# Kernel optimization log

Measured on AMD Instinct MI355X. Metric: run time of the kernel, lower is better.

The kernel has to match this reference:

```python
import jax, jax.numpy as jnp
import numpy as np

SHAPE = (192, 224, 192)
COG = np.array([96.0, 112.0, 96.0], dtype=np.float32)


def _rotation(a):
    # a: (3,) angles. R = Rx @ Ry @ Rz, matching _compute_rotation.
    one = jnp.ones(()); zero = jnp.zeros(())
    cx, sx = jnp.cos(a[0]), jnp.sin(a[0])
    cy, sy = jnp.cos(a[1]), jnp.sin(a[1])
    cz, sz = jnp.cos(a[2]), jnp.sin(a[2])
    Rx = jnp.stack([jnp.stack([one, zero, zero]),
                    jnp.stack([zero, cx, -sx]),
                    jnp.stack([zero, sx, cx])])
    Ry = jnp.stack([jnp.stack([cy, zero, sy]),
                    jnp.stack([zero, one, zero]),
                    jnp.stack([-sy, zero, cy])])
    Rz = jnp.stack([jnp.stack([cz, -sz, zero]),
                    jnp.stack([sz, cz, zero]),
                    jnp.stack([zero, zero, one])])
    return Rx @ Ry @ Rz


def _compose_matrix(angle, translation, scaling, ref_v2r, flo_v2r):
    # factors are all 1; scaling param is log-scale -> exp
    ang = angle[0]
    sc = jnp.exp(scaling[0])
    tx = translation[0]
    eye = jnp.eye(4, dtype=angle.dtype)
    cog = jnp.asarray(COG, dtype=angle.dtype)
    T_center = eye.at[:3, 3].set(-cog)
    T_center_inv = eye.at[:3, 3].set(cog)
    T_sc = jnp.diag(jnp.concatenate([sc, jnp.ones((1,), angle.dtype)]))
    T_trans = eye.at[:3, 3].set(tx)
    T_rot = eye.at[:3, :3].set(_rotation(ang))
    T_rig = T_center_inv @ T_trans @ T_rot @ T_sc @ T_center
    return jnp.linalg.inv(flo_v2r) @ T_rig @ ref_v2r


def _trilinear(vol, di, dj, dk):
    # fast_3D_interp_torch, mode='linear': zero outside, clamp ceil at border
    D, H, W = vol.shape
    ok = (di > 0) & (dj > 0) & (dk > 0) & (di <= D - 1) & (dj <= H - 1) & (dk <= W - 1)
    fi = jnp.clip(jnp.floor(di), 0, D - 1)
    fj = jnp.clip(jnp.floor(dj), 0, H - 1)
    fk = jnp.clip(jnp.floor(dk), 0, W - 1)
    wi = di - fi; wj = dj - fj; wk = dk - fk
    fi = fi.astype(jnp.int32); fj = fj.astype(jnp.int32); fk = fk.astype(jnp.int32)
    ci = jnp.minimum(fi + 1, D - 1)
    cj = jnp.minimum(fj + 1, H - 1)
    ck = jnp.minimum(fk + 1, W - 1)
    c000 = vol[fi, fj, fk]; c100 = vol[ci, fj, fk]
    c010 = vol[fi, cj, fk]; c110 = vol[ci, cj, fk]
    c001 = vol[fi, fj, ck]; c101 = vol[ci, fj, ck]
    c011 = vol[fi, cj, ck]; c111 = vol[ci, cj, ck]
    out = ((c000 * (1 - wi) + c100 * wi) * (1 - wj) + (c010 * (1 - wi) + c110 * wi) * wj) * (1 - wk) \
        + ((c001 * (1 - wi) + c101 * wi) * (1 - wj) + (c011 * (1 - wi) + c111 * wi) * wj) * wk
    return jnp.where(ok, out, jnp.zeros((), vol.dtype))


def reference(image_targ, angle, translation, scaling, ref_v2r, flo_v2r):
    T = _compose_matrix(angle, translation, scaling, ref_v2r, flo_v2r)
    D, H, W = SHAPE
    ii, jj, kk = jnp.meshgrid(jnp.arange(D, dtype=image_targ.dtype),
                              jnp.arange(H, dtype=image_targ.dtype),
                              jnp.arange(W, dtype=image_targ.dtype), indexing='ij')
    di = T[0, 0] * ii + T[0, 1] * jj + T[0, 2] * kk + T[0, 3]
    dj = T[1, 0] * ii + T[1, 1] * jj + T[1, 2] * kk + T[1, 3]
    dk = T[2, 0] * ii + T[2, 1] * jj + T[2, 2] * kk + T[2, 3]
    out = _trilinear(image_targ[0, 0], di, dj, dk)
    return out[None, None]


def setup_inputs() -> dict:
    key = jax.random.key(0)
    k1, k2, k3, k4 = jax.random.split(key, 4)
    D, H, W = SHAPE
    image_targ = jax.random.normal(k1, (1, 1, D, H, W), dtype=jnp.float32)
    angle = jax.random.normal(k2, (1, 3), dtype=jnp.float32) * 0.05
    translation = jax.random.normal(k3, (1, 3), dtype=jnp.float32) * 2.0
    scaling = jax.random.normal(k4, (1, 3), dtype=jnp.float32) * 0.02
    ref_v2r = jnp.eye(4, dtype=jnp.float32)
    flo_v2r = jnp.eye(4, dtype=jnp.float32)
    return {"image_targ": image_targ, "angle": angle, "translation": translation,
            "scaling": scaling, "ref_v2r": ref_v2r, "flo_v2r": flo_v2r}
```

## Files before the change

### kernel.cpp

```cpp
#include <hip/hip_runtime.h>
#include <hip/hip_bf16.h>
#include <math.h>

#define D_DIM 192
#define H_DIM 224
#define W_DIM 192


__device__ inline void mm4(const float* A, const float* B, float* C) {
    for (int r = 0; r < 4; ++r)
        for (int c = 0; c < 4; ++c) {
            float s = 0.f;
            for (int t = 0; t < 4; ++t) s += A[r * 4 + t] * B[t * 4 + c];
            C[r * 4 + c] = s;
        }
}

__device__ inline void inv4(const float* Ain, float* out) {
    float a[4][8];
    for (int r = 0; r < 4; ++r) {
        for (int c = 0; c < 4; ++c) a[r][c] = Ain[r * 4 + c];
        for (int c = 0; c < 4; ++c) a[r][4 + c] = (r == c) ? 1.f : 0.f;
    }
    for (int col = 0; col < 4; ++col) {
        int piv = col;
        float best = fabsf(a[col][col]);
        for (int r = col + 1; r < 4; ++r) {
            float v = fabsf(a[r][col]);
            if (v > best) { best = v; piv = r; }
        }
        if (piv != col) {
            for (int c = 0; c < 8; ++c) {
                float t = a[col][c]; a[col][c] = a[piv][c]; a[piv][c] = t;
            }
        }
        float inv = 1.f / a[col][col];
        for (int c = 0; c < 8; ++c) a[col][c] *= inv;
        for (int r = 0; r < 4; ++r) {
            if (r == col) continue;
            float f = a[r][col];
            for (int c = 0; c < 8; ++c) a[r][c] -= f * a[col][c];
        }
    }
    for (int r = 0; r < 4; ++r)
        for (int c = 0; c < 4; ++c) out[r * 4 + c] = a[r][4 + c];
}

__global__ void compute_T_kernel(const float* __restrict__ ang,
                                 const float* __restrict__ tr,
                                 const float* __restrict__ scl,
                                 const float* __restrict__ ref_v2r,
                                 const float* __restrict__ flo_v2r,
                                 float* __restrict__ Tout) {
    if (threadIdx.x != 0 || blockIdx.x != 0) return;

    const float cogx = 96.f, cogy = 112.f, cogz = 96.f;

    float cx = cosf(ang[0]), sx = sinf(ang[0]);
    float cy = cosf(ang[1]), sy = sinf(ang[1]);
    float cz = cosf(ang[2]), sz = sinf(ang[2]);

    float Rx[9] = {1, 0, 0, 0, cx, -sx, 0, sx, cx};
    float Ry[9] = {cy, 0, sy, 0, 1, 0, -sy, 0, cy};
    float Rz[9] = {cz, -sz, 0, sz, cz, 0, 0, 0, 1};
    float Ryz[9], R[9];
    for (int r = 0; r < 3; ++r)
        for (int c = 0; c < 3; ++c) {
            float s = 0.f;
            for (int t = 0; t < 3; ++t) s += Ry[r * 3 + t] * Rz[t * 3 + c];
            Ryz[r * 3 + c] = s;
        }
    for (int r = 0; r < 3; ++r)
        for (int c = 0; c < 3; ++c) {
            float s = 0.f;
            for (int t = 0; t < 3; ++t) s += Rx[r * 3 + t] * Ryz[t * 3 + c];
            R[r * 3 + c] = s;
        }

    float s0 = expf(scl[0]), s1 = expf(scl[1]), s2 = expf(scl[2]);

    float Tc[16]    = {1,0,0,-cogx, 0,1,0,-cogy, 0,0,1,-cogz, 0,0,0,1};
    float Tci[16]   = {1,0,0, cogx, 0,1,0, cogy, 0,0,1, cogz, 0,0,0,1};
    float Tsc[16]   = {s0,0,0,0, 0,s1,0,0, 0,0,s2,0, 0,0,0,1};
    float Ttr[16]   = {1,0,0,tr[0], 0,1,0,tr[1], 0,0,1,tr[2], 0,0,0,1};
    float Trot[16]  = {R[0],R[1],R[2],0, R[3],R[4],R[5],0, R[6],R[7],R[8],0, 0,0,0,1};

    float m1[16], m2[16], m3[16], Trig[16];
    mm4(Tci, Ttr, m1);
    mm4(m1, Trot, m2);
    mm4(m2, Tsc, m3);
    mm4(m3, Tc, Trig);

    float floinv[16], m4[16], T[16];
    inv4(flo_v2r, floinv);
    mm4(floinv, Trig, m4);
    mm4(m4, ref_v2r, T);

    for (int q = 0; q < 12; ++q) Tout[q] = T[q];
}


__global__ __launch_bounds__(W_DIM) void resample_kernel(
    const float* __restrict__ vol,
    const float* __restrict__ T,
    float* __restrict__ out) {
    const int k = threadIdx.x;
    const int j = blockIdx.y;
    const int i = blockIdx.z;

    const float fi = (float)i, fj = (float)j, fk = (float)k;

    const float t00 = T[0],  t01 = T[1],  t02 = T[2],  t03 = T[3];
    const float t10 = T[4],  t11 = T[5],  t12 = T[6],  t13 = T[7];
    const float t20 = T[8],  t21 = T[9],  t22 = T[10], t23 = T[11];

    const float di = t00 * fi + t01 * fj + t02 * fk + t03;
    const float dj = t10 * fi + t11 * fj + t12 * fk + t13;
    const float dk = t20 * fi + t21 * fj + t22 * fk + t23;

    const bool ok = (di > 0.f) & (dj > 0.f) & (dk > 0.f) &
                    (di <= (float)(D_DIM - 1)) &
                    (dj <= (float)(H_DIM - 1)) &
                    (dk <= (float)(W_DIM - 1));

    float ffi = fminf(fmaxf(floorf(di), 0.f), (float)(D_DIM - 1));
    float ffj = fminf(fmaxf(floorf(dj), 0.f), (float)(H_DIM - 1));
    float ffk = fminf(fmaxf(floorf(dk), 0.f), (float)(W_DIM - 1));

    const float wi = di - ffi;
    const float wj = dj - ffj;
    const float wk = dk - ffk;

    const int i0 = (int)ffi, j0 = (int)ffj, k0 = (int)ffk;
    const int i1 = min(i0 + 1, D_DIM - 1);
    const int j1 = min(j0 + 1, H_DIM - 1);
    const int k1 = min(k0 + 1, W_DIM - 1);

    const int base00 = (i0 * H_DIM + j0) * W_DIM;
    const int base01 = (i0 * H_DIM + j1) * W_DIM;
    const int base10 = (i1 * H_DIM + j0) * W_DIM;
    const int base11 = (i1 * H_DIM + j1) * W_DIM;

    const float c000 = vol[base00 + k0];
    const float c100 = vol[base10 + k0];
    const float c010 = vol[base01 + k0];
    const float c110 = vol[base11 + k0];
    const float c001 = vol[base00 + k1];
    const float c101 = vol[base10 + k1];
    const float c011 = vol[base01 + k1];
    const float c111 = vol[base11 + k1];

    const float omwi = 1.f - wi, omwj = 1.f - wj, omwk = 1.f - wk;

    const float v = ((c000 * omwi + c100 * wi) * omwj +
                     (c010 * omwi + c110 * wi) * wj) * omwk +
                    ((c001 * omwi + c101 * wi) * omwj +
                     (c011 * omwi + c111 * wi) * wj) * wk;

    out[(i * H_DIM + j) * W_DIM + k] = ok ? v : 0.f;
}


extern "C" void kernel_launch(void* const* d_in, const int* in_sizes, int n_in,
                              void* d_out, int out_size, void* d_ws, size_t ws_size,
                              hipStream_t stream) {
    const float* image_targ  = (const float*)d_in[0];
    const float* angle       = (const float*)d_in[1];
    const float* translation = (const float*)d_in[2];
    const float* scaling     = (const float*)d_in[3];
    const float* ref_v2r     = (const float*)d_in[4];
    const float* flo_v2r     = (const float*)d_in[5];
    float* out = (float*)d_out;
    float* Tmat = (float*)d_ws;

    compute_T_kernel<<<1, 1, 0, stream>>>(angle, translation, scaling,
                                          ref_v2r, flo_v2r, Tmat);

    dim3 block(W_DIM, 1, 1);
    dim3 grid(1, H_DIM, D_DIM);
    resample_kernel<<<grid, block, 0, stream>>>(image_targ, Tmat, out);
}
```

Baseline: 140.6 us.

## Process four rows per block with XCD-aware block remapping and nontemporal stores

Each block now handles four consecutive j-rows, issuing all 32 gather loads before the interpolation math so more memory requests are in flight per thread. Block indices are remapped so consecutive spatial chunks land on the same XCD, which is meant to improve L2 locality for neighbouring gather footprints. Output writes use nontemporal stores to avoid polluting cache. Register pressure rises and the total block count drops by four times.

```diff
diff --git a/kernel.cpp b/kernel.cpp
--- a/kernel.cpp
+++ b/kernel.cpp
@@ -5,6 +5,8 @@
 #define D_DIM 192
 #define H_DIM 224
 #define W_DIM 192
+#define ROWS_PER_BLOCK 4
+#define NUM_XCD 8
 
 
 __device__ inline void mm4(const float* A, const float* B, float* C) {
@@ -79,11 +81,11 @@
 
     float s0 = expf(scl[0]), s1 = expf(scl[1]), s2 = expf(scl[2]);
 
-    float Tc[16]    = {1,0,0,-cogx, 0,1,0,-cogy, 0,0,1,-cogz, 0,0,0,1};
-    float Tci[16]   = {1,0,0, cogx, 0,1,0, cogy, 0,0,1, cogz, 0,0,0,1};
-    float Tsc[16]   = {s0,0,0,0, 0,s1,0,0, 0,0,s2,0, 0,0,0,1};
-    float Ttr[16]   = {1,0,0,tr[0], 0,1,0,tr[1], 0,0,1,tr[2], 0,0,0,1};
-    float Trot[16]  = {R[0],R[1],R[2],0, R[3],R[4],R[5],0, R[6],R[7],R[8],0, 0,0,0,1};
+    float Tc[16]   = {1,0,0,-cogx, 0,1,0,-cogy, 0,0,1,-cogz, 0,0,0,1};
+    float Tci[16]  = {1,0,0, cogx, 0,1,0, cogy, 0,0,1, cogz, 0,0,0,1};
+    float Tsc[16]  = {s0,0,0,0, 0,s1,0,0, 0,0,s2,0, 0,0,0,1};
+    float Ttr[16]  = {1,0,0,tr[0], 0,1,0,tr[1], 0,0,1,tr[2], 0,0,0,1};
+    float Trot[16] = {R[0],R[1],R[2],0, R[3],R[4],R[5],0, R[6],R[7],R[8],0, 0,0,0,1};
 
     float m1[16], m2[16], m3[16], Trig[16];
     mm4(Tci, Ttr, m1);
@@ -104,60 +106,77 @@
     const float* __restrict__ vol,
     const float* __restrict__ T,
     float* __restrict__ out) {
+
+    constexpr int NBLK = (D_DIM * H_DIM) / ROWS_PER_BLOCK;
+    constexpr int PER_XCD = NBLK / NUM_XCD;
+
+    const int b = blockIdx.x;
+    const int xcd = b & (NUM_XCD - 1);
+    const int q = b >> 3;
+    const int sb = xcd * PER_XCD + q;
+    const int row_base = sb * ROWS_PER_BLOCK;
+    const int i = row_base / H_DIM;
+    const int jbase = row_base % H_DIM;
     const int k = threadIdx.x;
-    const int j = blockIdx.y;
-    const int i = blockIdx.z;
-
-    const float fi = (float)i, fj = (float)j, fk = (float)k;
 
     const float t00 = T[0],  t01 = T[1],  t02 = T[2],  t03 = T[3];
     const float t10 = T[4],  t11 = T[5],  t12 = T[6],  t13 = T[7];
     const float t20 = T[8],  t21 = T[9],  t22 = T[10], t23 = T[11];
 
-    const float di = t00 * fi + t01 * fj + t02 * fk + t03;
-    const float dj = t10 * fi + t11 * fj + t12 * fk + t13;
-    const float dk = t20 * fi + t21 * fj + t22 * fk + t23;
-
-    const bool ok = (di > 0.f) & (dj > 0.f) & (dk > 0.f) &
-                    (di <= (float)(D_DIM - 1)) &
-                    (dj <= (float)(H_DIM - 1)) &
-                    (dk <= (float)(W_DIM - 1));
-
-    float ffi = fminf(fmaxf(floorf(di), 0.f), (float)(D_DIM - 1));
-    float ffj = fminf(fmaxf(floorf(dj), 0.f), (float)(H_DIM - 1));
-    float ffk = fminf(fmaxf(floorf(dk), 0.f), (float)(W_DIM - 1));
-
-    const float wi = di - ffi;
-    const float wj = dj - ffj;
-    const float wk = dk - ffk;
-
-    const int i0 = (int)ffi, j0 = (int)ffj, k0 = (int)ffk;
-    const int i1 = min(i0 + 1, D_DIM - 1);
-    const int j1 = min(j0 + 1, H_DIM - 1);
-    const int k1 = min(k0 + 1, W_DIM - 1);
-
-    const int base00 = (i0 * H_DIM + j0) * W_DIM;
-    const int base01 = (i0 * H_DIM + j1) * W_DIM;
-    const int base10 = (i1 * H_DIM + j0) * W_DIM;
-    const int base11 = (i1 * H_DIM + j1) * W_DIM;
-
-    const float c000 = vol[base00 + k0];
-    const float c100 = vol[base10 + k0];
-    const float c010 = vol[base01 + k0];
-    const float c110 = vol[base11 + k0];
-    const float c001 = vol[base00 + k1];
-    const float c101 = vol[base10 + k1];
-    const float c011 = vol[base01 + k1];
-    const float c111 = vol[base11 + k1];
-
-    const float omwi = 1.f - wi, omwj = 1.f - wj, omwk = 1.f - wk;
-
-    const float v = ((c000 * omwi + c100 * wi) * omwj +
-                     (c010 * omwi + c110 * wi) * wj) * omwk +
-                    ((c001 * omwi + c101 * wi) * omwj +
-                     (c011 * omwi + c111 * wi) * wj) * wk;
-
-    out[(i * H_DIM + j) * W_DIM + k] = ok ? v : 0.f;
+    const float fi = (float)i, fk = (float)k;
+
+    float c[ROWS_PER_BLOCK][8];
+    float wi[ROWS_PER_BLOCK], wj[ROWS_PER_BLOCK], wk[ROWS_PER_BLOCK];
+    bool okr[ROWS_PER_BLOCK];
+
+#pragma unroll
+    for (int r = 0; r < ROWS_PER_BLOCK; ++r) {
+        const float fj = (float)(jbase + r);
+        const float di = t00 * fi + t01 * fj + t02 * fk + t03;
+        const float dj = t10 * fi + t11 * fj + t12 * fk + t13;
+        const float dk = t20 * fi + t21 * fj + t22 * fk + t23;
+
+        okr[r] = (di > 0.f) & (dj > 0.f) & (dk > 0.f) &
+                 (di <= (float)(D_DIM - 1)) &
+                 (dj <= (float)(H_DIM - 1)) &
+                 (dk <= (float)(W_DIM - 1));
+
+        float ffi = fminf(fmaxf(floorf(di), 0.f), (float)(D_DIM - 1));
+        float ffj = fminf(fmaxf(floorf(dj), 0.f), (float)(H_DIM - 1));
+        float ffk = fminf(fmaxf(floorf(dk), 0.f), (float)(W_DIM - 1));
+
+        wi[r] = di - ffi; wj[r] = dj - ffj; wk[r] = dk - ffk;
+
+        const int i0 = (int)ffi, j0 = (int)ffj, k0 = (int)ffk;
+        const int i1 = min(i0 + 1, D_DIM - 1);
+        const int j1 = min(j0 + 1, H_DIM - 1);
+        const int k1 = min(k0 + 1, W_DIM - 1);
+
+        const int base00 = (i0 * H_DIM + j0) * W_DIM;
+        const int base01 = (i0 * H_DIM + j1) * W_DIM;
+        const int base10 = (i1 * H_DIM + j0) * W_DIM;
+        const int base11 = (i1 * H_DIM + j1) * W_DIM;
+
+        c[r][0] = vol[base00 + k0];
+        c[r][1] = vol[base10 + k0];
+        c[r][2] = vol[base01 + k0];
+        c[r][3] = vol[base11 + k0];
+        c[r][4] = vol[base00 + k1];
+        c[r][5] = vol[base10 + k1];
+        c[r][6] = vol[base01 + k1];
+        c[r][7] = vol[base11 + k1];
+    }
+
+#pragma unroll
+    for (int r = 0; r < ROWS_PER_BLOCK; ++r) {
+        const float omwi = 1.f - wi[r], omwj = 1.f - wj[r], omwk = 1.f - wk[r];
+        const float v = ((c[r][0] * omwi + c[r][1] * wi[r]) * omwj +
+                         (c[r][2] * omwi + c[r][3] * wi[r]) * wj[r]) * omwk +
+                        ((c[r][4] * omwi + c[r][5] * wi[r]) * omwj +
+                         (c[r][6] * omwi + c[r][7] * wi[r]) * wj[r]) * wk[r];
+        const float res = okr[r] ? v : 0.f;
+        __builtin_nontemporal_store(res, &out[(i * H_DIM + (jbase + r)) * W_DIM + k]);
+    }
 }
 
 
@@ -176,7 +195,6 @@
     compute_T_kernel<<<1, 1, 0, stream>>>(angle, translation, scaling,
                                           ref_v2r, flo_v2r, Tmat);
 
-    dim3 block(W_DIM, 1, 1);
-    dim3 grid(1, H_DIM, D_DIM);
-    resample_kernel<<<grid, block, 0, stream>>>(image_targ, Tmat, out);
-}
+    const int nblk = (D_DIM * H_DIM) / ROWS_PER_BLOCK;
+    resample_kernel<<<nblk, W_DIM, 0, stream>>>(image_targ, Tmat, out);
+}
```

After: 142.8 us. Within noise of the previous version (+1.6%).

## Tile resampling into 3D blocks with shared-memory source staging and XCD-aware mapping

Applied to the files above, without the earlier changes.

Replaces the one-row-per-block trilinear resample with 8x8x16 output tiles of 256 threads. Each tile's source bounding box is computed from its corners and staged into LDS, so the eight neighbour gathers read shared memory instead of global memory, with a global-memory fallback when the box does not fit. Blocks are remapped so neighbouring tiles land on the same XCD for L2 locality, and outputs use nontemporal stores. This adds LDS staging cost and a barrier per tile, and loads some source voxels the tile never uses.

```diff
diff --git a/kernel.cpp b/kernel.cpp
--- a/kernel.cpp
+++ b/kernel.cpp
@@ -5,6 +5,13 @@
 #define D_DIM 192
 #define H_DIM 224
 #define W_DIM 192
+#define IT 8
+#define JT 8
+#define KT 16
+#define BLOCK 256
+#define NUM_XCD 8
+#define NKP 24
+#define MAXROWS 256
 
 
 __device__ inline void mm4(const float* A, const float* B, float* C) {
@@ -79,11 +86,11 @@
 
     float s0 = expf(scl[0]), s1 = expf(scl[1]), s2 = expf(scl[2]);
 
-    float Tc[16]    = {1,0,0,-cogx, 0,1,0,-cogy, 0,0,1,-cogz, 0,0,0,1};
-    float Tci[16]   = {1,0,0, cogx, 0,1,0, cogy, 0,0,1, cogz, 0,0,0,1};
-    float Tsc[16]   = {s0,0,0,0, 0,s1,0,0, 0,0,s2,0, 0,0,0,1};
-    float Ttr[16]   = {1,0,0,tr[0], 0,1,0,tr[1], 0,0,1,tr[2], 0,0,0,1};
-    float Trot[16]  = {R[0],R[1],R[2],0, R[3],R[4],R[5],0, R[6],R[7],R[8],0, 0,0,0,1};
+    float Tc[16]   = {1,0,0,-cogx, 0,1,0,-cogy, 0,0,1,-cogz, 0,0,0,1};
+    float Tci[16]  = {1,0,0, cogx, 0,1,0, cogy, 0,0,1, cogz, 0,0,0,1};
+    float Tsc[16]  = {s0,0,0,0, 0,s1,0,0, 0,0,s2,0, 0,0,0,1};
+    float Ttr[16]  = {1,0,0,tr[0], 0,1,0,tr[1], 0,0,1,tr[2], 0,0,0,1};
+    float Trot[16] = {R[0],R[1],R[2],0, R[3],R[4],R[5],0, R[6],R[7],R[8],0, 0,0,0,1};
 
     float m1[16], m2[16], m3[16], Trig[16];
     mm4(Tci, Ttr, m1);
@@ -100,64 +107,139 @@
 }
 
 
-__global__ __launch_bounds__(W_DIM) void resample_kernel(
+__global__ __launch_bounds__(BLOCK) void resample_kernel(
     const float* __restrict__ vol,
     const float* __restrict__ T,
     float* __restrict__ out) {
-    const int k = threadIdx.x;
-    const int j = blockIdx.y;
-    const int i = blockIdx.z;
-
-    const float fi = (float)i, fj = (float)j, fk = (float)k;
+
+    constexpr int NTI = D_DIM / IT;
+    constexpr int NTJ = H_DIM / JT;
+    constexpr int NTK = W_DIM / KT;
+    constexpr int NBLK = NTI * NTJ * NTK;
+    constexpr int PER_XCD = NBLK / NUM_XCD;
+
+    __shared__ float S[MAXROWS * NKP];
+
+    const int b = blockIdx.x;
+    const int xcd = b & (NUM_XCD - 1);
+    const int sb = xcd * PER_XCD + (b >> 3);
+    const int it = sb / (NTJ * NTK);
+    const int rem = sb - it * (NTJ * NTK);
+    const int jt = rem / NTK;
+    const int kt = rem - jt * NTK;
+    const int ibase = it * IT, jbase = jt * JT, kbase = kt * KT;
+
+    const int tid = threadIdx.x;
+    const int kx = tid & 15;
+    const int jy = (tid >> 4) & 7;
+    const int ig = tid >> 7;
 
     const float t00 = T[0],  t01 = T[1],  t02 = T[2],  t03 = T[3];
     const float t10 = T[4],  t11 = T[5],  t12 = T[6],  t13 = T[7];
     const float t20 = T[8],  t21 = T[9],  t22 = T[10], t23 = T[11];
 
-    const float di = t00 * fi + t01 * fj + t02 * fk + t03;
-    const float dj = t10 * fi + t11 * fj + t12 * fk + t13;
-    const float dk = t20 * fi + t21 * fj + t22 * fk + t23;
-
-    const bool ok = (di > 0.f) & (dj > 0.f) & (dk > 0.f) &
-                    (di <= (float)(D_DIM - 1)) &
-                    (dj <= (float)(H_DIM - 1)) &
-                    (dk <= (float)(W_DIM - 1));
-
-    float ffi = fminf(fmaxf(floorf(di), 0.f), (float)(D_DIM - 1));
-    float ffj = fminf(fmaxf(floorf(dj), 0.f), (float)(H_DIM - 1));
-    float ffk = fminf(fmaxf(floorf(dk), 0.f), (float)(W_DIM - 1));
-
-    const float wi = di - ffi;
-    const float wj = dj - ffj;
-    const float wk = dk - ffk;
-
-    const int i0 = (int)ffi, j0 = (int)ffj, k0 = (int)ffk;
-    const int i1 = min(i0 + 1, D_DIM - 1);
-    const int j1 = min(j0 + 1, H_DIM - 1);
-    const int k1 = min(k0 + 1, W_DIM - 1);
-
-    const int base00 = (i0 * H_DIM + j0) * W_DIM;
-    const int base01 = (i0 * H_DIM + j1) * W_DIM;
-    const int base10 = (i1 * H_DIM + j0) * W_DIM;
-    const int base11 = (i1 * H_DIM + j1) * W_DIM;
-
-    const float c000 = vol[base00 + k0];
-    const float c100 = vol[base10 + k0];
-    const float c010 = vol[base01 + k0];
-    const float c110 = vol[base11 + k0];
-    const float c001 = vol[base00 + k1];
-    const float c101 = vol[base10 + k1];
-    const float c011 = vol[base01 + k1];
-    const float c111 = vol[base11 + k1];
-
-    const float omwi = 1.f - wi, omwj = 1.f - wj, omwk = 1.f - wk;
-
-    const float v = ((c000 * omwi + c100 * wi) * omwj +
-                     (c010 * omwi + c110 * wi) * wj) * omwk +
-                    ((c001 * omwi + c101 * wi) * omwj +
-                     (c011 * omwi + c111 * wi) * wj) * wk;
-
-    out[(i * H_DIM + j) * W_DIM + k] = ok ? v : 0.f;
+    float dil = 1e30f, dih = -1e30f;
+    float djl = 1e30f, djh = -1e30f;
+    float dkl = 1e30f, dkh = -1e30f;
+#pragma unroll
+    for (int c = 0; c < 8; ++c) {
+        const float ci = (float)(ibase + ((c & 1) ? IT - 1 : 0));
+        const float cj = (float)(jbase + ((c & 2) ? JT - 1 : 0));
+        const float ck = (float)(kbase + ((c & 4) ? KT - 1 : 0));
+        const float di = t00 * ci + t01 * cj + t02 * ck + t03;
+        const float dj = t10 * ci + t11 * cj + t12 * ck + t13;
+        const float dk = t20 * ci + t21 * cj + t22 * ck + t23;
+        dil = fminf(dil, di); dih = fmaxf(dih, di);
+        djl = fminf(djl, dj); djh = fmaxf(djh, dj);
+        dkl = fminf(dkl, dk); dkh = fmaxf(dkh, dk);
+    }
+    const int i0b = min(max((int)floorf(dil) - 1, 0), D_DIM - 1);
+    const int iHi = min(max((int)floorf(dih) + 2, 0), D_DIM - 1);
+    const int j0b = min(max((int)floorf(djl) - 1, 0), H_DIM - 1);
+    const int jHi = min(max((int)floorf(djh) + 2, 0), H_DIM - 1);
+    const int k0b = min(max((int)floorf(dkl) - 1, 0), W_DIM - 1);
+    const int kHi = min(max((int)floorf(dkh) + 2, 0), W_DIM - 1);
+    const int ni = iHi - i0b + 1;
+    const int nj = jHi - j0b + 1;
+    const int nk = kHi - k0b + 1;
+    const int R = ni * nj;
+    const bool fits = (R <= MAXROWS) && (nk <= NKP) && (nj >= 8);
+
+    if (fits) {
+        const int bk = tid & 31;
+        const int tr = tid >> 5;
+        int r = tr;
+        int bj = tr;
+        int rowg = i0b * H_DIM + (j0b + bj);
+        const int passes = (R + 7) >> 3;
+        for (int p = 0; p < passes; ++p) {
+            if (r < R && bk < nk) {
+                S[r * NKP + bk] = vol[rowg * W_DIM + k0b + bk];
+            }
+            r += 8;
+            bj += 8; rowg += 8;
+            if (bj >= nj) { bj -= nj; rowg += H_DIM - nj; }
+        }
+        __syncthreads();
+    }
+
+    const float fjv = (float)(jbase + jy);
+    const float fkv = (float)(kbase + kx);
+#pragma unroll
+    for (int v = 0; v < 4; ++v) {
+        const int iz = v * 2 + ig;
+        const float fiv = (float)(ibase + iz);
+
+        const float di = t00 * fiv + t01 * fjv + t02 * fkv + t03;
+        const float dj = t10 * fiv + t11 * fjv + t12 * fkv + t13;
+        const float dk = t20 * fiv + t21 * fjv + t22 * fkv + t23;
+
+        const bool ok = (di > 0.f) & (dj > 0.f) & (dk > 0.f) &
+                        (di <= (float)(D_DIM - 1)) &
+                        (dj <= (float)(H_DIM - 1)) &
+                        (dk <= (float)(W_DIM - 1));
+
+        float ffi = fminf(fmaxf(floorf(di), 0.f), (float)(D_DIM - 1));
+        float ffj = fminf(fmaxf(floorf(dj), 0.f), (float)(H_DIM - 1));
+        float ffk = fminf(fmaxf(floorf(dk), 0.f), (float)(W_DIM - 1));
+
+        const float wi = di - ffi, wj = dj - ffj, wk = dk - ffk;
+
+        const int i0 = (int)ffi, j0 = (int)ffj, k0 = (int)ffk;
+        const int i1 = min(i0 + 1, D_DIM - 1);
+        const int j1 = min(j0 + 1, H_DIM - 1);
+        const int k1 = min(k0 + 1, W_DIM - 1);
+
+        float c000, c100, c010, c110, c001, c101, c011, c111;
+        if (fits) {
+            const int a   = ((i0 - i0b) * nj + (j0 - j0b)) * NKP + (k0 - k0b);
+            const int rD  = (i1 - i0) * nj * NKP;
+            const int cD  = (j1 - j0) * NKP;
+            const int dk1 = k1 - k0;
+            c000 = S[a];            c001 = S[a + dk1];
+            c010 = S[a + cD];       c011 = S[a + cD + dk1];
+            c100 = S[a + rD];       c101 = S[a + rD + dk1];
+            c110 = S[a + rD + cD];  c111 = S[a + rD + cD + dk1];
+        } else {
+            const int b00 = (i0 * H_DIM + j0) * W_DIM;
+            const int b01 = (i0 * H_DIM + j1) * W_DIM;
+            const int b10 = (i1 * H_DIM + j0) * W_DIM;
+            const int b11 = (i1 * H_DIM + j1) * W_DIM;
+            c000 = vol[b00 + k0]; c100 = vol[b10 + k0];
+            c010 = vol[b01 + k0]; c110 = vol[b11 + k0];
+            c001 = vol[b00 + k1]; c101 = vol[b10 + k1];
+            c011 = vol[b01 + k1]; c111 = vol[b11 + k1];
+        }
+
+        const float omwi = 1.f - wi, omwj = 1.f - wj, omwk = 1.f - wk;
+        const float val = ((c000 * omwi + c100 * wi) * omwj +
+                           (c010 * omwi + c110 * wi) * wj) * omwk +
+                          ((c001 * omwi + c101 * wi) * omwj +
+                           (c011 * omwi + c111 * wi) * wj) * wk;
+        const float res = ok ? val : 0.f;
+        __builtin_nontemporal_store(
+            res, &out[((ibase + iz) * H_DIM + (jbase + jy)) * W_DIM + kbase + kx]);
+    }
 }
 
 
@@ -176,7 +258,6 @@
     compute_T_kernel<<<1, 1, 0, stream>>>(angle, translation, scaling,
                                           ref_v2r, flo_v2r, Tmat);
 
-    dim3 block(W_DIM, 1, 1);
-    dim3 grid(1, H_DIM, D_DIM);
-    resample_kernel<<<grid, block, 0, stream>>>(image_targ, Tmat, out);
-}
+    const int nblk = (D_DIM / IT) * (H_DIM / JT) * (W_DIM / KT);
+    resample_kernel<<<nblk, BLOCK, 0, stream>>>(image_targ, Tmat, out);
+}
```

Measured after the change: 141.3 us. About the same (+0.5%).
